# Optimization experiments

Hardware: AMD Instinct MI355X
Metric: run time of the kernel (lower is better)

## Reference

```python
import jax, jax.numpy as jnp
import numpy as np

B, T_V, T_T, C, H = 4, 8192, 77, 1024, 16
D = C // H  # head_dim = 64


def setup_inputs() -> dict:
    key = jax.random.key(0)
    ks = jax.random.split(key, 6)
    s = 1.0 / np.sqrt(C)
    return {
        "video_features": jax.random.normal(ks[0], (B, T_V, C), jnp.float32),
        "text_features": jax.random.normal(ks[1], (B, T_T, C), jnp.float32),
        "Wq": jax.random.normal(ks[2], (C, C), jnp.float32) * s,
        "Wk": jax.random.normal(ks[3], (C, C), jnp.float32) * s,
        "Wv": jax.random.normal(ks[4], (C, C), jnp.float32) * s,
        "Wo": jax.random.normal(ks[5], (C, C), jnp.float32) * s,
    }


def reference(video_features, text_features, Wq, Wk, Wv, Wo):
    # nn.Linear(no bias): y = x @ W.T
    q = (video_features @ Wq.T).reshape(B, T_V, H, D).transpose(0, 2, 1, 3)  # [B,H,Tv,D]
    k = (text_features @ Wk.T).reshape(B, T_T, H, D).transpose(0, 2, 1, 3)   # [B,H,Tt,D]
    v = (text_features @ Wv.T).reshape(B, T_T, H, D).transpose(0, 2, 1, 3)   # [B,H,Tt,D]
    scores = jnp.einsum("bhqd,bhkd->bhqk", q, k) / jnp.sqrt(jnp.float32(D))
    attn = jax.nn.softmax(scores, axis=-1)
    out = jnp.einsum("bhqk,bhkd->bhqd", attn, v)
    out = out.transpose(0, 2, 1, 3).reshape(B, T_V, C)
    return out @ Wo.T
```

## Files before the change

kernel.cpp:

```cpp
#include <hip/hip_runtime.h>
#include <hip/hip_bf16.h>


typedef __attribute__((ext_vector_type(8))) short bf16x8;
typedef __attribute__((ext_vector_type(4))) float f32x4;
typedef __attribute__((ext_vector_type(8))) unsigned short u16x8;
typedef __attribute__((ext_vector_type(4))) unsigned short u16x4;

typedef const __attribute__((address_space(1))) void gv_t;
typedef __attribute__((address_space(3))) void lv_t;

static __device__ __forceinline__ unsigned short f2bf(float f) {
    union { float f; unsigned u; } v; v.f = f;
    unsigned r = v.u + 0x7FFFu + ((v.u >> 16) & 1u);
    return (unsigned short)(r >> 16);
}

constexpr int Bn = 4, TVn = 8192, TTn = 77, Cn = 1024, Hn = 16;

__device__ __forceinline__ void cvt8_body(const float* __restrict__ in,
                                          unsigned short* __restrict__ out, int i) {
    const float4* p = reinterpret_cast<const float4*>(in) + (size_t)i * 2;
    float4 a = p[0], b = p[1];
    u16x8 o = { f2bf(a.x), f2bf(a.y), f2bf(a.z), f2bf(a.w),
                f2bf(b.x), f2bf(b.y), f2bf(b.z), f2bf(b.w) };
    *reinterpret_cast<u16x8*>(out + (size_t)i * 8) = o;
}

__global__ __launch_bounds__(256)
void k_prep(const float* __restrict__ video, const float* __restrict__ text,
            const float* __restrict__ Wq, const float* __restrict__ Wk,
            const float* __restrict__ Wv, const float* __restrict__ Wo,
            unsigned short* __restrict__ wq_b, unsigned short* __restrict__ wo_b,
            unsigned short* __restrict__ kbuf, unsigned short* __restrict__ vbuf,
            unsigned short* __restrict__ vid_b) {
    __shared__ unsigned short As[128 * 32];
    __shared__ unsigned short Bs[128 * 32];
    const int tid = threadIdx.x;
    int bid = blockIdx.x;

    if (bid >= 48) {
        bid -= 48;
        if (bid < 512)       cvt8_body(Wq, wq_b, bid * 256 + tid);
        else if (bid < 1024) cvt8_body(Wo, wo_b, (bid - 512) * 256 + tid);
        else                 cvt8_body(video, vid_b, (bid - 1024) * 256 + tid);
        return;
    }
    const int bx = bid % 3, by = (bid / 3) % 8, bz = bid / 24;
    const float* W = bz ? Wv : Wk;
    unsigned short* out = bz ? vbuf : kbuf;
    const int M = Bn * TTn;
    const int lane = tid & 63, wv = tid >> 6;
    const int m0 = bx * 128, n0 = by * 128;
    const int wr = (wv >> 1) * 64, wc = (wv & 1) * 64;
    const int lr = lane & 15, lk = (lane >> 4) * 8, lg = lane >> 4;
    f32x4 acc[4][4] = {};
    for (int kk = 0; kk < 1024; kk += 32) {
        #pragma unroll
        for (int it = 0; it < 4; ++it) {
            int li = it * 256 + tid;
            int row = li >> 3, c4 = (li & 7) * 4;
            int gr = m0 + row;
            float4 v = make_float4(0.f, 0.f, 0.f, 0.f);
            if (gr < M) v = *reinterpret_cast<const float4*>(text + (size_t)gr * 1024 + kk + c4);
            u16x4 o = { f2bf(v.x), f2bf(v.y), f2bf(v.z), f2bf(v.w) };
            *reinterpret_cast<u16x4*>(&As[row * 32 + c4]) = o;
        }
        #pragma unroll
        for (int it = 0; it < 4; ++it) {
            int li = it * 256 + tid;
            int row = li >> 3, c4 = (li & 7) * 4;
            float4 v = *reinterpret_cast<const float4*>(W + (size_t)(n0 + row) * 1024 + kk + c4);
            u16x4 o = { f2bf(v.x), f2bf(v.y), f2bf(v.z), f2bf(v.w) };
            *reinterpret_cast<u16x4*>(&Bs[row * 32 + c4]) = o;
        }
        __syncthreads();
        bf16x8 af[4], bfv[4];
        #pragma unroll
        for (int m = 0; m < 4; ++m)
            af[m] = *reinterpret_cast<const bf16x8*>(&As[(wr + m * 16 + lr) * 32 + lk]);
        #pragma unroll
        for (int n = 0; n < 4; ++n)
            bfv[n] = *reinterpret_cast<const bf16x8*>(&Bs[(wc + n * 16 + lr) * 32 + lk]);
        #pragma unroll
        for (int m = 0; m < 4; ++m)
            #pragma unroll
            for (int n = 0; n < 4; ++n)
                acc[m][n] = __builtin_amdgcn_mfma_f32_16x16x32_bf16(af[m], bfv[n], acc[m][n], 0, 0, 0);
        __syncthreads();
    }
    #pragma unroll
    for (int m = 0; m < 4; ++m)
        #pragma unroll
        for (int n = 0; n < 4; ++n)
            #pragma unroll
            for (int r = 0; r < 4; ++r) {
                int grow = m0 + wr + m * 16 + lg * 4 + r;
                if (grow < M) {
                    int gcol = n0 + wc + n * 16 + lr;
                    out[(size_t)grow * 1024 + gcol] = f2bf(acc[m][n][r]);
                }
            }
}

__device__ __forceinline__ void stage_h(const unsigned short* __restrict__ src, int grow0, int kcol0,
                                        unsigned short* lds, int tid) {
    #pragma unroll
    for (int j = 0; j < 2; ++j) {
        const int row = j * 64 + (tid >> 3);
        const int sseg = (tid & 7) ^ (row & 7);
        const unsigned short* g = src + (size_t)(grow0 + row) * 1024 + kcol0 + sseg * 8;
        unsigned short* d = lds + j * 4096 + (tid >> 6) * 512;
        __builtin_amdgcn_global_load_lds((gv_t*)g, (lv_t*)d, 16, 0, 0);
    }
}

template<int BUF, int MQ>
__device__ __forceinline__ void p8_loadA(bf16x8 (&af)[4][2],
        const unsigned short (&As)[2][2][128][64], int wm, int lr, int lg) {
    #pragma unroll
    for (int m4 = 0; m4 < 4; ++m4)
        #pragma unroll
        for (int kk = 0; kk < 2; ++kk) {
            const int rl = MQ * 64 + m4 * 16 + lr;
            af[m4][kk] = *reinterpret_cast<const bf16x8*>(
                &As[BUF][wm][rl][((kk * 4 + lg) ^ (rl & 7)) * 8]);
        }
}

template<int BUF, int NQ>
__device__ __forceinline__ void p8_loadB(bf16x8 (&bg)[2][2],
        const unsigned short (&Bs)[2][2][128][64], int wn, int lr, int lg) {
    #pragma unroll
    for (int n2 = 0; n2 < 2; ++n2)
        #pragma unroll
        for (int kk = 0; kk < 2; ++kk) {
            const int nrow = wn * 64 + (NQ * 2 + n2) * 16 + lr;
            bg[n2][kk] = *reinterpret_cast<const bf16x8*>(
                &Bs[BUF][nrow >> 7][nrow & 127][((kk * 4 + lg) ^ (nrow & 7)) * 8]);
        }
}

template<int MQ, int NQ>
__device__ __forceinline__ void p8_mfma(f32x4 (&acc)[8][4],
        const bf16x8 (&af)[4][2], const bf16x8 (&bg)[2][2]) {
    #pragma unroll
    for (int m4 = 0; m4 < 4; ++m4)
        #pragma unroll
        for (int n2 = 0; n2 < 2; ++n2)
            #pragma unroll
            for (int kk = 0; kk < 2; ++kk)
                acc[MQ * 4 + m4][NQ * 2 + n2] = __builtin_amdgcn_mfma_f32_16x16x32_bf16(
                    af[m4][kk], bg[n2][kk], acc[MQ * 4 + m4][NQ * 2 + n2], 0, 0, 0);
}

#define P8_PRE()                                              \
    __builtin_amdgcn_s_barrier();                             \
    __builtin_amdgcn_s_setprio(1);

template<int OUT_MODE>
__global__ __launch_bounds__(512, 1)
void k_g256p8(const unsigned short* __restrict__ A, const unsigned short* __restrict__ Wb,
              void* __restrict__ outp) {
    __shared__ unsigned short As[2][2][128][64];
    __shared__ unsigned short Bs[2][2][128][64];
    const int tid = threadIdx.x, lane = tid & 63;
    const int wid = tid >> 6, wm = wid >> 2, wn = wid & 3;
    const int orig = blockIdx.x;
    const int work = (orig & 7) * 64 + (orig >> 3);
    const int m0 = (work >> 2) * 256, n0 = (work & 3) * 256;
    const int lr = lane & 15, lg = lane >> 4;

    f32x4 acc[8][4] = {};
    bf16x8 af[4][2], bg0[2][2], bg1[2][2];

    stage_h(A,  m0,       0,  &As[0][0][0][0], tid);
    stage_h(A,  m0 + 128, 0,  &As[0][1][0][0], tid);
    stage_h(Wb, n0,       0,  &Bs[0][0][0][0], tid);
    stage_h(Wb, n0 + 128, 0,  &Bs[0][1][0][0], tid);
    stage_h(Wb, n0,       64, &Bs[1][0][0][0], tid);
    stage_h(Wb, n0 + 128, 64, &Bs[1][1][0][0], tid);
    asm volatile("s_waitcnt vmcnt(4)" ::: "memory");
    __builtin_amdgcn_s_barrier();

    for (int t = 0; t < 16; t += 2) {
        const int k1 = (t + 1) * 64;
        const bool s2 = (t + 2) < 16, s3 = (t + 3) < 16;
        p8_loadA<0, 0>(af, As, wm, lr, lg);
        p8_loadB<0, 0>(bg0, Bs, wn, lr, lg);
        stage_h(A, m0, k1, &As[1][0][0][0], tid);
        P8_PRE(); p8_mfma<0, 0>(acc, af, bg0);
        __builtin_amdgcn_s_setprio(0); __builtin_amdgcn_s_barrier();
        p8_loadB<0, 1>(bg1, Bs, wn, lr, lg);
        stage_h(A, m0 + 128, k1, &As[1][1][0][0], tid);
        P8_PRE(); p8_mfma<0, 1>(acc, af, bg1);
        __builtin_amdgcn_s_setprio(0); __builtin_amdgcn_s_barrier();
        p8_loadA<0, 1>(af, As, wm, lr, lg);
        if (s2) stage_h(Wb, n0, k1 + 64, &Bs[0][0][0][0], tid);
        P8_PRE(); p8_mfma<1, 1>(acc, af, bg1);
        __builtin_amdgcn_s_setprio(0); __builtin_amdgcn_s_barrier();
        if (s2) stage_h(Wb, n0 + 128, k1 + 64, &Bs[0][1][0][0], tid);
        P8_PRE(); p8_mfma<1, 0>(acc, af, bg0);
        __builtin_amdgcn_s_setprio(0);
        if (s2) { asm volatile("s_waitcnt vmcnt(4)" ::: "memory"); }
        else    { asm volatile("s_waitcnt vmcnt(0)" ::: "memory"); }
        __builtin_amdgcn_s_barrier();
        p8_loadA<1, 0>(af, As, wm, lr, lg);
        p8_loadB<1, 0>(bg0, Bs, wn, lr, lg);
        if (s2) stage_h(A, m0, k1 + 64, &As[0][0][0][0], tid);
        P8_PRE(); p8_mfma<0, 0>(acc, af, bg0);
        __builtin_amdgcn_s_setprio(0); __builtin_amdgcn_s_barrier();
        p8_loadB<1, 1>(bg1, Bs, wn, lr, lg);
        if (s2) stage_h(A, m0 + 128, k1 + 64, &As[0][1][0][0], tid);
        P8_PRE(); p8_mfma<0, 1>(acc, af, bg1);
        __builtin_amdgcn_s_setprio(0); __builtin_amdgcn_s_barrier();
        p8_loadA<1, 1>(af, As, wm, lr, lg);
        if (s3) stage_h(Wb, n0, k1 + 128, &Bs[1][0][0][0], tid);
        P8_PRE(); p8_mfma<1, 1>(acc, af, bg1);
        __builtin_amdgcn_s_setprio(0); __builtin_amdgcn_s_barrier();
        if (s3) stage_h(Wb, n0 + 128, k1 + 128, &Bs[1][1][0][0], tid);
        P8_PRE(); p8_mfma<1, 0>(acc, af, bg0);
        __builtin_amdgcn_s_setprio(0);
        if (s3) { asm volatile("s_waitcnt vmcnt(4)" ::: "memory"); }
        else    { asm volatile("s_waitcnt vmcnt(0)" ::: "memory"); }
        __builtin_amdgcn_s_barrier();
    }

    #pragma unroll
    for (int mf = 0; mf < 8; ++mf)
        #pragma unroll
        for (int nf = 0; nf < 4; ++nf)
            #pragma unroll
            for (int r = 0; r < 4; ++r) {
                int grow = m0 + wm * 128 + mf * 16 + lg * 4 + r;
                int gcol = n0 + wn * 64 + nf * 16 + lr;
                if (OUT_MODE == 0) {
                    float v = acc[mf][nf][r];
                    float o = __shfl_xor(v, 1);
                    if (!(lane & 1)) {
                        float* out = (float*)outp;
                        float2 pv; pv.x = v; pv.y = o;
                        *reinterpret_cast<float2*>(out + (size_t)grow * 1024 + gcol) = pv;
                    }
                } else {
                    unsigned short bv = f2bf(acc[mf][nf][r]);
                    unsigned ov = __shfl_xor((unsigned)bv, 1);
                    if (!(lane & 1)) {
                        unsigned short* out = (unsigned short*)outp;
                        size_t off = (OUT_MODE == 1)
                            ? (size_t)grow * 1024 + gcol
                            : ((size_t)(gcol >> 6) * (Bn * TVn) + grow) * 64 + (gcol & 63);
                        *reinterpret_cast<unsigned*>(out + off) = (unsigned)bv | (ov << 16);
                    }
                }
            }
}

__global__ __launch_bounds__(512)
void k_attn5(const unsigned short* __restrict__ qh,
             const unsigned short* __restrict__ kb,
             const unsigned short* __restrict__ vb,
             unsigned short* __restrict__ aout) {
    constexpr int VP = 104;
    __shared__ unsigned short vt_s[64 * VP];
    const int tid = threadIdx.x, lane = tid & 63, wv = tid >> 6;
    const int m0 = blockIdx.x * 256;
    const int h = blockIdx.y, b = blockIdx.z;
    const size_t qhbase = ((size_t)h * (Bn * TVn) + (size_t)b * TVn + m0) * 64;
    const size_t kvbase = (size_t)b * TTn * Cn + h * 64;
    const int lr = lane & 15, lg = lane >> 4;

    for (int li = tid; li < 640; li += 512) {
        int t = li >> 3, sg = li & 7;
        u16x8 v = {0, 0, 0, 0, 0, 0, 0, 0};
        if (t < 77) v = *reinterpret_cast<const u16x8*>(vb + kvbase + (size_t)t * Cn + sg * 8);
        #pragma unroll
        for (int i = 0; i < 8; ++i) vt_s[(sg * 8 + i) * VP + t] = v[i];
    }
    for (int li = tid; li < 1024; li += 512) {
        int d = li >> 4, t = 80 + (li & 15);
        vt_s[d * VP + t] = 0;
    }

    f32x4 sc[2][5] = {};
    #pragma unroll
    for (int ks = 0; ks < 2; ++ks) {
        bf16x8 qa[2], kf[5];
        #pragma unroll
        for (int mf = 0; mf < 2; ++mf)
            qa[mf] = *reinterpret_cast<const bf16x8*>(
                qh + qhbase + (size_t)(wv * 32 + mf * 16 + lr) * 64 + ks * 32 + lg * 8);
        #pragma unroll
        for (int nf = 0; nf < 5; ++nf) {
            int t = nf * 16 + lr; if (t > 76) t = 76;
            kf[nf] = *reinterpret_cast<const bf16x8*>(
                kb + kvbase + (size_t)t * Cn + ks * 32 + lg * 8);
        }
        #pragma unroll
        for (int mf = 0; mf < 2; ++mf)
            #pragma unroll
            for (int nf = 0; nf < 5; ++nf)
                sc[mf][nf] = __builtin_amdgcn_mfma_f32_16x16x32_bf16(kf[nf], qa[mf], sc[mf][nf], 0, 0, 0);
    }

    unsigned pk[2][6][2];
    constexpr float CEXP = 0.125f * 1.44269504088896340736f;
    #pragma unroll
    for (int mf = 0; mf < 2; ++mf) {
        float mx = -1e30f;
        #pragma unroll
        for (int nf = 0; nf < 5; ++nf)
            #pragma unroll
            for (int r = 0; r < 4; ++r)
                if (!(nf == 4 && r >= 1)) mx = fmaxf(mx, sc[mf][nf][r]);
                else if (lg != 3)         mx = fmaxf(mx, sc[mf][nf][r]);
        mx = fmaxf(mx, __shfl_xor(mx, 16));
        mx = fmaxf(mx, __shfl_xor(mx, 32));
        float p[5][4];
        float sum = 0.f;
        #pragma unroll
        for (int nf = 0; nf < 5; ++nf)
            #pragma unroll
            for (int r = 0; r < 4; ++r) {
                bool valid = !(nf == 4 && lg == 3 && r >= 1);
                float pv = valid ? exp2f((sc[mf][nf][r] - mx) * CEXP) : 0.f;
                p[nf][r] = pv;
                sum += pv;
            }
        sum += __shfl_xor(sum, 16);
        sum += __shfl_xor(sum, 32);
        float inv = 1.f / sum;
        #pragma unroll
        for (int nf = 0; nf < 5; ++nf) {
            pk[mf][nf][0] = (unsigned)f2bf(p[nf][0] * inv) | ((unsigned)f2bf(p[nf][1] * inv) << 16);
            pk[mf][nf][1] = (unsigned)f2bf(p[nf][2] * inv) | ((unsigned)f2bf(p[nf][3] * inv) << 16);
        }
        pk[mf][5][0] = 0; pk[mf][5][1] = 0;
    }

    __syncthreads();

    f32x4 ovv[2][4] = {};
    const int sel = lg >> 1;
    const int srcA = ((lg & 1) * 2) * 16 + lr;
    const int srcB = ((lg & 1) * 2 + 1) * 16 + lr;
    #pragma unroll
    for (int ks = 0; ks < 3; ++ks) {
        bf16x8 vf[4];
        #pragma unroll
        for (int nf = 0; nf < 4; ++nf)
            vf[nf] = *reinterpret_cast<const bf16x8*>(
                &vt_s[(nf * 16 + lr) * VP + ks * 32 + lg * 8]);
        #pragma unroll
        for (int mf = 0; mf < 2; ++mf) {
            unsigned w0l = __shfl(pk[mf][ks * 2 + 0][0], srcA);
            unsigned w0h = __shfl(pk[mf][ks * 2 + 1][0], srcA);
            unsigned w1l = __shfl(pk[mf][ks * 2 + 0][1], srcA);
            unsigned w1h = __shfl(pk[mf][ks * 2 + 1][1], srcA);
            unsigned w2l = __shfl(pk[mf][ks * 2 + 0][0], srcB);
            unsigned w2h = __shfl(pk[mf][ks * 2 + 1][0], srcB);
            unsigned w3l = __shfl(pk[mf][ks * 2 + 0][1], srcB);
            unsigned w3h = __shfl(pk[mf][ks * 2 + 1][1], srcB);
            union { uint4 u; bf16x8 v; } pa;
            pa.u.x = sel ? w0h : w0l;
            pa.u.y = sel ? w1h : w1l;
            pa.u.z = sel ? w2h : w2l;
            pa.u.w = sel ? w3h : w3l;
            #pragma unroll
            for (int nf = 0; nf < 4; ++nf)
                ovv[mf][nf] = __builtin_amdgcn_mfma_f32_16x16x32_bf16(pa.v, vf[nf], ovv[mf][nf], 0, 0, 0);
        }
    }

    #pragma unroll
    for (int mf = 0; mf < 2; ++mf)
        #pragma unroll
        for (int nf = 0; nf < 4; ++nf)
            #pragma unroll
            for (int r = 0; r < 4; ++r) {
                unsigned short bv = f2bf(ovv[mf][nf][r]);
                unsigned o = __shfl_xor((unsigned)bv, 1);
                if (!(lane & 1)) {
                    int row = m0 + wv * 32 + mf * 16 + lg * 4 + r;
                    int col = h * 64 + nf * 16 + lr;
                    *reinterpret_cast<unsigned*>(aout + ((size_t)b * TVn + row) * Cn + col) =
                        (unsigned)bv | (o << 16);
                }
            }
}

extern "C" void kernel_launch(void* const* d_in, const int* in_sizes, int n_in,
                              void* d_out, int out_size, void* d_ws, size_t ws_size,
                              hipStream_t stream) {
    const float* video = (const float*)d_in[0];
    const float* text  = (const float*)d_in[1];
    const float* Wq = (const float*)d_in[2];
    const float* Wk = (const float*)d_in[3];
    const float* Wv = (const float*)d_in[4];
    const float* Wo = (const float*)d_in[5];
    float* out = (float*)d_out;

    char* ws = (char*)d_ws;
    unsigned short* wq_b  = (unsigned short*)(ws);
    unsigned short* wo_b  = (unsigned short*)(ws + (2u << 20));
    unsigned short* kbuf  = (unsigned short*)(ws + (4u << 20));
    unsigned short* vbuf  = (unsigned short*)(ws + (5u << 20));
    unsigned short* qhbuf = (unsigned short*)(ws + (6u << 20));
    unsigned short* vid_b = (unsigned short*)(ws + (70u << 20));

    k_prep<<<48 + 512 + 512 + 16384, 256, 0, stream>>>(
        video, text, Wq, Wk, Wv, Wo, wq_b, wo_b, kbuf, vbuf, vid_b);

    k_g256p8<2><<<512, 512, 0, stream>>>(vid_b, wq_b, (void*)qhbuf);

    dim3 ga(TVn / 256, Hn, Bn);
    k_attn5<<<ga, 512, 0, stream>>>(qhbuf, kbuf, vbuf, vid_b);

    k_g256p8<0><<<512, 512, 0, stream>>>(vid_b, wo_b, (void*)out);
}
```

Baseline: 302.2 us.

## Load GEMM weight operand directly from global into registers, triple-buffer A in LDS

The weight (B) tiles are no longer staged through LDS. Each wave now reads its B fragments straight from global memory into registers at the start of every k-step. The freed LDS holds a third A buffer, so A is triple-buffered and the loop drops its two-step unroll for a rotating buffer index. This is meant to cut LDS traffic and barrier pressure for B. The cost is exposed global/L2 latency on B loads that are consumed almost immediately, strided per-row reads that coalesce poorly, and repeated B fetches across the waves that share columns.

```diff
diff --git a/kernel.cpp b/kernel.cpp
--- a/kernel.cpp
+++ b/kernel.cpp
@@ -115,29 +115,29 @@
     }
 }
 
-template<int BUF, int MQ>
+template<int MQ>
 __device__ __forceinline__ void p8_loadA(bf16x8 (&af)[4][2],
-        const unsigned short (&As)[2][2][128][64], int wm, int lr, int lg) {
+        const unsigned short* Abuf, int wm, int lr, int lg) {
     #pragma unroll
     for (int m4 = 0; m4 < 4; ++m4)
         #pragma unroll
         for (int kk = 0; kk < 2; ++kk) {
             const int rl = MQ * 64 + m4 * 16 + lr;
             af[m4][kk] = *reinterpret_cast<const bf16x8*>(
-                &As[BUF][wm][rl][((kk * 4 + lg) ^ (rl & 7)) * 8]);
-        }
-}
-
-template<int BUF, int NQ>
-__device__ __forceinline__ void p8_loadB(bf16x8 (&bg)[2][2],
-        const unsigned short (&Bs)[2][2][128][64], int wn, int lr, int lg) {
+                Abuf + ((size_t)(wm * 128 + rl)) * 64 + ((kk * 4 + lg) ^ (rl & 7)) * 8);
+        }
+}
+
+__device__ __forceinline__ void p8_loadBg(bf16x8 (&bg0)[2][2], bf16x8 (&bg1)[2][2],
+        const unsigned short* __restrict__ bbase, int k0, int lg) {
     #pragma unroll
     for (int n2 = 0; n2 < 2; ++n2)
         #pragma unroll
         for (int kk = 0; kk < 2; ++kk) {
-            const int nrow = wn * 64 + (NQ * 2 + n2) * 16 + lr;
-            bg[n2][kk] = *reinterpret_cast<const bf16x8*>(
-                &Bs[BUF][nrow >> 7][nrow & 127][((kk * 4 + lg) ^ (nrow & 7)) * 8]);
+            bg0[n2][kk] = *reinterpret_cast<const bf16x8*>(
+                bbase + (size_t)n2 * 16 * 1024 + k0 + kk * 32 + lg * 8);
+            bg1[n2][kk] = *reinterpret_cast<const bf16x8*>(
+                bbase + (size_t)(2 + n2) * 16 * 1024 + k0 + kk * 32 + lg * 8);
         }
 }
 
@@ -162,68 +162,53 @@
 __global__ __launch_bounds__(512, 1)
 void k_g256p8(const unsigned short* __restrict__ A, const unsigned short* __restrict__ Wb,
               void* __restrict__ outp) {
-    __shared__ unsigned short As[2][2][128][64];
-    __shared__ unsigned short Bs[2][2][128][64];
+    __shared__ unsigned short As[3][2][128][64];
     const int tid = threadIdx.x, lane = tid & 63;
     const int wid = tid >> 6, wm = wid >> 2, wn = wid & 3;
     const int orig = blockIdx.x;
     const int work = (orig & 7) * 64 + (orig >> 3);
     const int m0 = (work >> 2) * 256, n0 = (work & 3) * 256;
     const int lr = lane & 15, lg = lane >> 4;
+    const unsigned short* bbase = Wb + (size_t)(n0 + wn * 64 + lr) * 1024;
+    unsigned short* As0 = &As[0][0][0][0];
 
     f32x4 acc[8][4] = {};
     bf16x8 af[4][2], bg0[2][2], bg1[2][2];
 
-    stage_h(A,  m0,       0,  &As[0][0][0][0], tid);
-    stage_h(A,  m0 + 128, 0,  &As[0][1][0][0], tid);
-    stage_h(Wb, n0,       0,  &Bs[0][0][0][0], tid);
-    stage_h(Wb, n0 + 128, 0,  &Bs[0][1][0][0], tid);
-    stage_h(Wb, n0,       64, &Bs[1][0][0][0], tid);
-    stage_h(Wb, n0 + 128, 64, &Bs[1][1][0][0], tid);
+    stage_h(A, m0,       0,  As0,                  tid);
+    stage_h(A, m0 + 128, 0,  As0 + 128 * 64,       tid);
+    stage_h(A, m0,       64, As0 + 2 * 128 * 64,   tid);
+    stage_h(A, m0 + 128, 64, As0 + 3 * 128 * 64,   tid);
     asm volatile("s_waitcnt vmcnt(4)" ::: "memory");
     __builtin_amdgcn_s_barrier();
 
-    for (int t = 0; t < 16; t += 2) {
-        const int k1 = (t + 1) * 64;
-        const bool s2 = (t + 2) < 16, s3 = (t + 3) < 16;
-        p8_loadA<0, 0>(af, As, wm, lr, lg);
-        p8_loadB<0, 0>(bg0, Bs, wn, lr, lg);
-        stage_h(A, m0, k1, &As[1][0][0][0], tid);
+    int bt = 0, bs = 2;
+    for (int t = 0; t < 16; ++t) {
+        const int k0 = t * 64;
+        const unsigned short* Abuf = As0 + (size_t)bt * (2 * 128 * 64);
+        unsigned short* Sbuf = As0 + (size_t)bs * (2 * 128 * 64);
+        const bool st = (t + 2) < 16;
+
+        p8_loadBg(bg0, bg1, bbase, k0, lg);
+
+        p8_loadA<0>(af, Abuf, wm, lr, lg);
+        if (st) stage_h(A, m0, k0 + 128, Sbuf, tid);
         P8_PRE(); p8_mfma<0, 0>(acc, af, bg0);
         __builtin_amdgcn_s_setprio(0); __builtin_amdgcn_s_barrier();
-        p8_loadB<0, 1>(bg1, Bs, wn, lr, lg);
-        stage_h(A, m0 + 128, k1, &As[1][1][0][0], tid);
+        if (st) stage_h(A, m0 + 128, k0 + 128, Sbuf + 128 * 64, tid);
         P8_PRE(); p8_mfma<0, 1>(acc, af, bg1);
         __builtin_amdgcn_s_setprio(0); __builtin_amdgcn_s_barrier();
-        p8_loadA<0, 1>(af, As, wm, lr, lg);
-        if (s2) stage_h(Wb, n0, k1 + 64, &Bs[0][0][0][0], tid);
+        p8_loadA<1>(af, Abuf, wm, lr, lg);
         P8_PRE(); p8_mfma<1, 1>(acc, af, bg1);
         __builtin_amdgcn_s_setprio(0); __builtin_amdgcn_s_barrier();
-        if (s2) stage_h(Wb, n0 + 128, k1 + 64, &Bs[0][1][0][0], tid);
         P8_PRE(); p8_mfma<1, 0>(acc, af, bg0);
         __builtin_amdgcn_s_setprio(0);
-        if (s2) { asm volatile("s_waitcnt vmcnt(4)" ::: "memory"); }
-        else    { asm volatile("s_waitcnt vmcnt(0)" ::: "memory"); }
+        if (t < 14) { asm volatile("s_waitcnt vmcnt(4)" ::: "memory"); }
+        else        { asm volatile("s_waitcnt vmcnt(0)" ::: "memory"); }
         __builtin_amdgcn_s_barrier();
-        p8_loadA<1, 0>(af, As, wm, lr, lg);
-        p8_loadB<1, 0>(bg0, Bs, wn, lr, lg);
-        if (s2) stage_h(A, m0, k1 + 64, &As[0][0][0][0], tid);
-        P8_PRE(); p8_mfma<0, 0>(acc, af, bg0);
-        __builtin_amdgcn_s_setprio(0); __builtin_amdgcn_s_barrier();
-        p8_loadB<1, 1>(bg1, Bs, wn, lr, lg);
-        if (s2) stage_h(A, m0 + 128, k1 + 64, &As[0][1][0][0], tid);
-        P8_PRE(); p8_mfma<0, 1>(acc, af, bg1);
-        __builtin_amdgcn_s_setprio(0); __builtin_amdgcn_s_barrier();
-        p8_loadA<1, 1>(af, As, wm, lr, lg);
-        if (s3) stage_h(Wb, n0, k1 + 128, &Bs[1][0][0][0], tid);
-        P8_PRE(); p8_mfma<1, 1>(acc, af, bg1);
-        __builtin_amdgcn_s_setprio(0); __builtin_amdgcn_s_barrier();
-        if (s3) stage_h(Wb, n0 + 128, k1 + 128, &Bs[1][1][0][0], tid);
-        P8_PRE(); p8_mfma<1, 0>(acc, af, bg0);
-        __builtin_amdgcn_s_setprio(0);
-        if (s3) { asm volatile("s_waitcnt vmcnt(4)" ::: "memory"); }
-        else    { asm volatile("s_waitcnt vmcnt(0)" ::: "memory"); }
-        __builtin_amdgcn_s_barrier();
+
+        bt = (bt == 2) ? 0 : bt + 1;
+        bs = (bs == 2) ? 0 : bs + 1;
     }
 
     #pragma unroll
```

After: 399.7 us. +32.3%, slower.
